# Optimization experiments

Hardware: AMD Instinct MI355X
Metric: run time of the kernel (lower is better)

Reference implementation:

```python
import jax, jax.numpy as jnp
import numpy as np

B = 512
INPUT_DIM = 1536
MAMBA_DIM = 1024
OUTPUT_DIM = 1024
D_STATE = 128
D_CONV = 4
EXPAND = 2
HEADDIM = 64
D_INNER = EXPAND * MAMBA_DIM          # 2048, == d_ssm
NHEADS = D_INNER // HEADDIM           # 32
CONV_DIM = D_INNER + 2 * D_STATE      # 2304
D_IN_PROJ = 2 * D_INNER + 2 * D_STATE + NHEADS  # 4384 (d_mlp = 0)
EPS = 1e-5


def rms_norm(x, g):
    return x * jax.lax.rsqrt(jnp.mean(x * x, axis=-1, keepdims=True) + EPS) * g


def setup_inputs() -> dict:
    key = jax.random.key(0)
    ks = jax.random.split(key, 16)
    def lin(k, fan_in, shape):
        return jax.random.normal(k, shape, jnp.float32) / np.sqrt(fan_in)
    return {
        "x": jax.random.normal(ks[0], (B, INPUT_DIM), jnp.float32),
        "conv_state": jax.random.normal(ks[1], (B, CONV_DIM, D_CONV), jnp.float32),
        "ssm_state": jax.random.normal(ks[2], (B, NHEADS, HEADDIM, D_STATE), jnp.float32),
        # NormedLinear in_proj (Linear + RMSNorm + SiLU)
        "w_in": lin(ks[3], INPUT_DIM, (INPUT_DIM, MAMBA_DIM)),
        "b_in": jnp.zeros((MAMBA_DIM,), jnp.float32),
        "g_in": jnp.ones((MAMBA_DIM,), jnp.float32),
        # Mamba2 params
        "W_inproj": lin(ks[4], MAMBA_DIM, (MAMBA_DIM, D_IN_PROJ)),
        "conv_w": lin(ks[5], D_CONV, (CONV_DIM, D_CONV)),
        "conv_b": jnp.zeros((CONV_DIM,), jnp.float32),
        "A_log": jnp.log(jax.random.uniform(ks[6], (NHEADS,), jnp.float32, 1.0, 16.0)),
        "dt_bias": 0.1 * jax.random.normal(ks[7], (NHEADS,), jnp.float32),
        "D": jnp.ones((NHEADS,), jnp.float32),
        "W_mamba_out": lin(ks[8], D_INNER, (D_INNER, MAMBA_DIM)),
        # outer out_proj Linear + RMSNorm
        "w_out": lin(ks[9], MAMBA_DIM, (MAMBA_DIM, OUTPUT_DIM)),
        "b_out": jnp.zeros((OUTPUT_DIM,), jnp.float32),
        "g_outnorm": jnp.ones((OUTPUT_DIM,), jnp.float32),
    }


def reference(x, conv_state, ssm_state, w_in, b_in, g_in, W_inproj, conv_w, conv_b,
              A_log, dt_bias, D, W_mamba_out, w_out, b_out, g_outnorm):
    # in_proj: Linear -> RMSNorm -> SiLU
    h = jax.nn.silu(rms_norm(x @ w_in + b_in, g_in))          # [B, MAMBA_DIM]
    zxbcdt = h @ W_inproj                                      # [B, D_IN_PROJ]
    z = zxbcdt[:, :D_INNER]                                    # [B, D_INNER]
    xbc = zxbcdt[:, D_INNER:D_INNER + CONV_DIM]                # [B, CONV_DIM]
    dt = zxbcdt[:, D_INNER + CONV_DIM:]                        # [B, NHEADS]
    # conv shift-and-sum
    conv_state_new = jnp.concatenate([conv_state[:, :, 1:], xbc[:, :, None]], axis=-1)
    xbc = jnp.sum(conv_state_new * conv_w[None], axis=-1) + conv_b
    xbc = jax.nn.silu(xbc)
    xh = xbc[:, :D_INNER].reshape(B, NHEADS, HEADDIM)          # [B, H, P]
    b = xbc[:, D_INNER:D_INNER + D_STATE]                      # [B, N]
    c = xbc[:, D_INNER + D_STATE:]                             # [B, N]
    # SSM step
    a = -jnp.exp(A_log)                                        # [H]
    dt = jax.nn.softplus(dt + dt_bias)                         # [B, H]
    da = jnp.exp(dt * a)                                       # [B, H]
    dbx = jnp.einsum('bh,bn,bhp->bhpn', dt, b, xh)
    ssm_state_new = ssm_state * da[:, :, None, None] + dbx     # [B, H, P, N]
    y = jnp.einsum('bhpn,bn->bhp', ssm_state_new, c)
    y = y + D[None, :, None] * xh
    y = y.reshape(B, D_INNER) * jax.nn.silu(z)
    y = y @ W_mamba_out                                        # [B, MAMBA_DIM]
    # outer projection + norm
    y = rms_norm(y @ w_out + b_out, g_outnorm)                 # [B, OUTPUT_DIM]
    return y, conv_state_new, ssm_state_new
```

## Files before the change

### kernel.cpp

```cpp
#include <hip/hip_runtime.h>
#include <hip/hip_bf16.h>

#define B_SZ      512
#define INPUT_DIM 1536
#define MAMBA_DIM 1024
#define OUT_DIM   1024
#define D_STATE   128
#define HEADDIM   64
#define D_INNER   2048
#define NHEADS    32
#define CONV_DIM  2304
#define D_IN_PROJ 4384

__device__ __forceinline__ float silu_precise(float x) {
    return x / (1.0f + expf(-x));
}

__global__ __launch_bounds__(256) void zero_kernel(float4* __restrict__ p, int n4)
{
    int i = blockIdx.x * 256 + threadIdx.x;
    const int stride = gridDim.x * 256;
    const float4 z = make_float4(0.f, 0.f, 0.f, 0.f);
    for (; i < n4; i += stride) p[i] = z;
}

__global__ __launch_bounds__(256) void sgemm_splitk_kernel(
    const float* __restrict__ A, const float* __restrict__ W,
    const float* __restrict__ bias, float* __restrict__ C,
    int M, int N, int K, int Kper)
{
    __shared__ float As[32][68];
    __shared__ float Bs[32][64];

    const int t   = threadIdx.x;
    const int bn0 = blockIdx.x * 64;
    const int bm0 = blockIdx.y * 64;
    const int kz0 = blockIdx.z * Kper;
    const int tr  = t >> 4;
    const int tc  = t & 15;

    float acc[4][4] = {};

    for (int kk = 0; kk < Kper; kk += 32) {
        const int k0 = kz0 + kk;
        #pragma unroll
        for (int i = 0; i < 2; ++i) {
            int idx = t + i * 256;
            int row = idx >> 3;
            int c4  = (idx & 7) * 4;
            float4 v = *(const float4*)(A + (size_t)(bm0 + row) * K + k0 + c4);
            As[c4 + 0][row] = v.x;
            As[c4 + 1][row] = v.y;
            As[c4 + 2][row] = v.z;
            As[c4 + 3][row] = v.w;
        }
        #pragma unroll
        for (int i = 0; i < 2; ++i) {
            int idx = t + i * 256;
            int kr  = idx >> 4;
            int c4  = (idx & 15) * 4;
            int n   = bn0 + c4;
            float4 v = make_float4(0.f, 0.f, 0.f, 0.f);
            if (n < N) v = *(const float4*)(W + (size_t)(k0 + kr) * N + n);
            *(float4*)&Bs[kr][c4] = v;
        }
        __syncthreads();

        #pragma unroll
        for (int k = 0; k < 32; ++k) {
            float4 a = *(const float4*)&As[k][tr * 4];
            float4 b = *(const float4*)&Bs[k][tc * 4];
            float av[4] = {a.x, a.y, a.z, a.w};
            float bv[4] = {b.x, b.y, b.z, b.w};
            #pragma unroll
            for (int i = 0; i < 4; ++i)
                #pragma unroll
                for (int j = 0; j < 4; ++j)
                    acc[i][j] += av[i] * bv[j];
        }
        __syncthreads();
    }

    const bool addb = (bias != nullptr) && (blockIdx.z == 0);
    #pragma unroll
    for (int i = 0; i < 4; ++i) {
        int m = bm0 + tr * 4 + i;
        #pragma unroll
        for (int j = 0; j < 4; ++j) {
            int n = bn0 + tc * 4 + j;
            if (n < N) {
                float v = acc[i][j];
                if (addb) v += bias[n];
                atomicAdd(&C[(size_t)m * N + n], v);
            }
        }
    }
}

template <bool SILU>
__global__ __launch_bounds__(256) void rmsnorm_kernel(
    const float* __restrict__ X, const float* __restrict__ g,
    float* __restrict__ Y)
{
    const int row = blockIdx.x;
    const float* x = X + (size_t)row * 1024;
    float4 v = *(const float4*)(x + threadIdx.x * 4);
    float ss = v.x * v.x + v.y * v.y + v.z * v.z + v.w * v.w;
    #pragma unroll
    for (int off = 32; off > 0; off >>= 1) ss += __shfl_down(ss, off);

    __shared__ float wsum[4];
    const int wid = threadIdx.x >> 6;
    if ((threadIdx.x & 63) == 0) wsum[wid] = ss;
    __syncthreads();
    const float tot = wsum[0] + wsum[1] + wsum[2] + wsum[3];
    const float rs = 1.0f / sqrtf(tot * (1.0f / 1024.0f) + 1e-5f);

    float4 gv = *(const float4*)(g + threadIdx.x * 4);
    float4 o;
    o.x = v.x * rs * gv.x;
    o.y = v.y * rs * gv.y;
    o.z = v.z * rs * gv.z;
    o.w = v.w * rs * gv.w;
    if (SILU) {
        o.x = silu_precise(o.x);
        o.y = silu_precise(o.y);
        o.z = silu_precise(o.z);
        o.w = silu_precise(o.w);
    }
    *(float4*)(Y + (size_t)row * 1024 + threadIdx.x * 4) = o;
}

__global__ __launch_bounds__(256) void conv_kernel(
    const float* __restrict__ conv_state, const float* __restrict__ zx,
    const float* __restrict__ conv_w, const float* __restrict__ conv_b,
    float* __restrict__ conv_state_out, float* __restrict__ xbc_out)
{
    const int gid = blockIdx.x * 256 + threadIdx.x;
    const int b = gid / CONV_DIM;
    const int c = gid - b * CONV_DIM;

    float4 cs = *(const float4*)(conv_state + (size_t)gid * 4);
    float xn = zx[(size_t)b * D_IN_PROJ + D_INNER + c];
    float4 w = *(const float4*)(conv_w + c * 4);

    float s = cs.y * w.x + cs.z * w.y + cs.w * w.z + xn * w.w + conv_b[c];
    float r = silu_precise(s);

    float4 o = make_float4(cs.y, cs.z, cs.w, xn);
    *(float4*)(conv_state_out + (size_t)gid * 4) = o;
    xbc_out[gid] = r;
}

__global__ __launch_bounds__(256) void ssm_kernel(
    const float* __restrict__ ssm_state, const float* __restrict__ xbc,
    const float* __restrict__ zx, const float* __restrict__ A_log,
    const float* __restrict__ dt_bias, const float* __restrict__ Dp,
    float* __restrict__ ssm_out, float* __restrict__ yz)
{
    const int h = blockIdx.x;
    const int b = blockIdx.y;
    const int t = threadIdx.x;
    const int lane_n = t & 31;
    const int n0 = lane_n * 4;
    const int pg = t >> 5;

    float dtv = zx[(size_t)b * D_IN_PROJ + (D_INNER + CONV_DIM) + h] + dt_bias[h];
    dtv = (dtv > 20.f) ? dtv : log1pf(expf(dtv));
    const float a  = -expf(A_log[h]);
    const float da = expf(dtv * a);
    const float dcoef = Dp[h];

    const float* xrow = xbc + (size_t)b * CONV_DIM;

    const float4 bb = *(const float4*)(xrow + D_INNER + n0);
    const float4 cc = *(const float4*)(xrow + D_INNER + D_STATE + n0);

    const size_t slab = ((size_t)b * NHEADS + h) * (HEADDIM * D_STATE);
    const float* sp = ssm_state + slab;
    float*       so = ssm_out   + slab;

    #pragma unroll
    for (int i = 0; i < 8; ++i) {
        const int p = pg + i * 8;
        const float xh = xrow[h * HEADDIM + p];
        const float coef = dtv * xh;

        const size_t off = (size_t)p * D_STATE + n0;
        float4 s = *(const float4*)(sp + off);
        float4 ns;
        ns.x = s.x * da + coef * bb.x;
        ns.y = s.y * da + coef * bb.y;
        ns.z = s.z * da + coef * bb.z;
        ns.w = s.w * da + coef * bb.w;
        *(float4*)(so + off) = ns;

        float y = ns.x * cc.x + ns.y * cc.y + ns.z * cc.z + ns.w * cc.w;
        y += __shfl_xor(y, 16);
        y += __shfl_xor(y, 8);
        y += __shfl_xor(y, 4);
        y += __shfl_xor(y, 2);
        y += __shfl_xor(y, 1);

        if (lane_n == 0) {
            float z = zx[(size_t)b * D_IN_PROJ + h * HEADDIM + p];
            float yv = y + dcoef * xh;
            yz[(size_t)b * D_INNER + h * HEADDIM + p] = yv * silu_precise(z);
        }
    }
}


extern "C" void kernel_launch(void* const* d_in, const int* in_sizes, int n_in,
                              void* d_out, int out_size, void* d_ws, size_t ws_size,
                              hipStream_t stream)
{
    const float* x          = (const float*)d_in[0];
    const float* conv_state = (const float*)d_in[1];
    const float* ssm_state  = (const float*)d_in[2];
    const float* w_in       = (const float*)d_in[3];
    const float* b_in       = (const float*)d_in[4];
    const float* g_in       = (const float*)d_in[5];
    const float* W_inproj   = (const float*)d_in[6];
    const float* conv_w     = (const float*)d_in[7];
    const float* conv_b     = (const float*)d_in[8];
    const float* A_log      = (const float*)d_in[9];
    const float* dt_bias    = (const float*)d_in[10];
    const float* Dp         = (const float*)d_in[11];
    const float* W_mamba_out= (const float*)d_in[12];
    const float* w_out      = (const float*)d_in[13];
    const float* b_out      = (const float*)d_in[14];
    const float* g_outnorm  = (const float*)d_in[15];

    float* out_y    = (float*)d_out;
    float* out_conv = out_y + (size_t)B_SZ * OUT_DIM;
    float* out_ssm  = out_conv + (size_t)B_SZ * CONV_DIM * 4;

    float* ws  = (float*)d_ws;
    float* t1  = ws;
    float* zx  = t1  + (size_t)B_SZ * MAMBA_DIM;
    float* u   = zx  + (size_t)B_SZ * D_IN_PROJ;
    float* t2  = u   + (size_t)B_SZ * MAMBA_DIM;
    float* h   = t2  + (size_t)B_SZ * MAMBA_DIM;
    float* xbc = h   + (size_t)B_SZ * MAMBA_DIM;
    float* yzb = xbc + (size_t)B_SZ * CONV_DIM;

    const int gemm_out_floats = B_SZ * (MAMBA_DIM + D_IN_PROJ + MAMBA_DIM + MAMBA_DIM);

    zero_kernel<<<2048, 256, 0, stream>>>((float4*)ws, gemm_out_floats / 4);

    sgemm_splitk_kernel<<<dim3(MAMBA_DIM / 64, B_SZ / 64, 8), 256, 0, stream>>>(
        x, w_in, b_in, t1, B_SZ, MAMBA_DIM, INPUT_DIM, INPUT_DIM / 8);
    rmsnorm_kernel<true><<<B_SZ, 256, 0, stream>>>(t1, g_in, h);
    sgemm_splitk_kernel<<<dim3((D_IN_PROJ + 63) / 64, B_SZ / 64, 4), 256, 0, stream>>>(
        h, W_inproj, nullptr, zx, B_SZ, D_IN_PROJ, MAMBA_DIM, MAMBA_DIM / 4);
    conv_kernel<<<(B_SZ * CONV_DIM) / 256, 256, 0, stream>>>(
        conv_state, zx, conv_w, conv_b, out_conv, xbc);
    ssm_kernel<<<dim3(NHEADS, B_SZ), 256, 0, stream>>>(
        ssm_state, xbc, zx, A_log, dt_bias, Dp, out_ssm, yzb);
    sgemm_splitk_kernel<<<dim3(MAMBA_DIM / 64, B_SZ / 64, 8), 256, 0, stream>>>(
        yzb, W_mamba_out, nullptr, u, B_SZ, MAMBA_DIM, D_INNER, D_INNER / 8);
    sgemm_splitk_kernel<<<dim3(OUT_DIM / 64, B_SZ / 64, 8), 256, 0, stream>>>(
        u, w_out, b_out, t2, B_SZ, OUT_DIM, MAMBA_DIM, MAMBA_DIM / 8);
    rmsnorm_kernel<false><<<B_SZ, 256, 0, stream>>>(t2, g_outnorm, out_y);
}
```

Before: 1.273 ms.

## Replace FP32 SIMT GEMMs with split-bf16x3 MFMA GEMMs on 128x128 tiles

Swaps the scalar FP32 split-K GEMM for a matrix-core kernel that splits each FP32 operand into bf16 hi/lo parts and uses three bf16 MFMAs per tile to approximate FP32 accuracy. Tiles grow from 64x64 to 128x128, with four waves each computing a 64x64 sub-tile. The aim is to move the four projection GEMMs from vector ALUs onto the MFMA units. In exchange, the hi/lo conversion adds ALU work, the B tile is stored transposed with scalar LDS writes that may cause bank conflicts, and the larger tiles give fewer blocks.

Result: faster. 1.102 ms (-13.4%).

```diff
diff --git a/kernel.cpp b/kernel.cpp
--- a/kernel.cpp
+++ b/kernel.cpp
@@ -1,5 +1,4 @@
 #include <hip/hip_runtime.h>
-#include <hip/hip_bf16.h>
 
 #define B_SZ      512
 #define INPUT_DIM 1536
@@ -12,8 +11,24 @@
 #define CONV_DIM  2304
 #define D_IN_PROJ 4384
 
+typedef short  short8 __attribute__((ext_vector_type(8)));
+typedef float  f32x4  __attribute__((ext_vector_type(4)));
+
 __device__ __forceinline__ float silu_precise(float x) {
     return x / (1.0f + expf(-x));
+}
+
+__device__ __forceinline__ ushort f2bf(float f) {
+    uint32_t u = __float_as_uint(f);
+    u += 0x7FFFu + ((u >> 16) & 1u);
+    return (ushort)(u >> 16);
+}
+__device__ __forceinline__ float bf2f(ushort h) {
+    return __uint_as_float(((uint32_t)h) << 16);
+}
+__device__ __forceinline__ void split_bf(float x, ushort& hi, ushort& lo) {
+    hi = f2bf(x);
+    lo = f2bf(x - bf2f(hi));
 }
 
 __global__ __launch_bounds__(256) void zero_kernel(float4* __restrict__ p, int n4)
@@ -24,74 +39,108 @@
     for (; i < n4; i += stride) p[i] = z;
 }
 
-__global__ __launch_bounds__(256) void sgemm_splitk_kernel(
+__global__ __launch_bounds__(256) void gemm_bf16x3_splitk(
     const float* __restrict__ A, const float* __restrict__ W,
     const float* __restrict__ bias, float* __restrict__ C,
     int M, int N, int K, int Kper)
 {
-    __shared__ float As[32][68];
-    __shared__ float Bs[32][64];
-
-    const int t   = threadIdx.x;
-    const int bn0 = blockIdx.x * 64;
-    const int bm0 = blockIdx.y * 64;
-    const int kz0 = blockIdx.z * Kper;
-    const int tr  = t >> 4;
-    const int tc  = t & 15;
-
-    float acc[4][4] = {};
+    __shared__ ushort As_hi[128][40];
+    __shared__ ushort As_lo[128][40];
+    __shared__ ushort Bs_hi[128][40];
+    __shared__ ushort Bs_lo[128][40];
+
+    const int t    = threadIdx.x;
+    const int bn0  = blockIdx.x * 128;
+    const int bm0  = blockIdx.y * 128;
+    const int kz0  = blockIdx.z * Kper;
+    const int wid  = t >> 6;
+    const int lane = t & 63;
+    const int wm   = (wid >> 1) * 64;
+    const int wn   = (wid & 1) * 64;
+    const int lr   = lane & 15;
+    const int lk   = lane >> 4;
+
+    f32x4 acc[4][4];
+    #pragma unroll
+    for (int i = 0; i < 4; ++i)
+        #pragma unroll
+        for (int j = 0; j < 4; ++j) {
+            f32x4 z = {0.f, 0.f, 0.f, 0.f};
+            acc[i][j] = z;
+        }
 
     for (int kk = 0; kk < Kper; kk += 32) {
         const int k0 = kz0 + kk;
-        #pragma unroll
-        for (int i = 0; i < 2; ++i) {
-            int idx = t + i * 256;
-            int row = idx >> 3;
-            int c4  = (idx & 7) * 4;
-            float4 v = *(const float4*)(A + (size_t)(bm0 + row) * K + k0 + c4);
-            As[c4 + 0][row] = v.x;
-            As[c4 + 1][row] = v.y;
-            As[c4 + 2][row] = v.z;
-            As[c4 + 3][row] = v.w;
-        }
-        #pragma unroll
-        for (int i = 0; i < 2; ++i) {
-            int idx = t + i * 256;
-            int kr  = idx >> 4;
-            int c4  = (idx & 15) * 4;
-            int n   = bn0 + c4;
+
+        #pragma unroll
+        for (int i = 0; i < 4; ++i) {
+            int c   = t + i * 256;
+            int row = c >> 3;
+            int k4  = (c & 7) * 4;
+            float4 v = *(const float4*)(A + (size_t)(bm0 + row) * K + k0 + k4);
+            ushort4 hi, lo;
+            split_bf(v.x, hi.x, lo.x);
+            split_bf(v.y, hi.y, lo.y);
+            split_bf(v.z, hi.z, lo.z);
+            split_bf(v.w, hi.w, lo.w);
+            *(ushort4*)&As_hi[row][k4] = hi;
+            *(ushort4*)&As_lo[row][k4] = lo;
+        }
+        #pragma unroll
+        for (int i = 0; i < 4; ++i) {
+            int c   = t + i * 256;
+            int kr  = c >> 5;
+            int n4  = (c & 31) * 4;
+            int n   = bn0 + n4;
             float4 v = make_float4(0.f, 0.f, 0.f, 0.f);
-            if (n < N) v = *(const float4*)(W + (size_t)(k0 + kr) * N + n);
-            *(float4*)&Bs[kr][c4] = v;
+            if (n + 4 <= N)
+                v = *(const float4*)(W + (size_t)(k0 + kr) * N + n);
+            ushort hi, lo;
+            split_bf(v.x, hi, lo); Bs_hi[n4 + 0][kr] = hi; Bs_lo[n4 + 0][kr] = lo;
+            split_bf(v.y, hi, lo); Bs_hi[n4 + 1][kr] = hi; Bs_lo[n4 + 1][kr] = lo;
+            split_bf(v.z, hi, lo); Bs_hi[n4 + 2][kr] = hi; Bs_lo[n4 + 2][kr] = lo;
+            split_bf(v.w, hi, lo); Bs_hi[n4 + 3][kr] = hi; Bs_lo[n4 + 3][kr] = lo;
         }
         __syncthreads();
 
-        #pragma unroll
-        for (int k = 0; k < 32; ++k) {
-            float4 a = *(const float4*)&As[k][tr * 4];
-            float4 b = *(const float4*)&Bs[k][tc * 4];
-            float av[4] = {a.x, a.y, a.z, a.w};
-            float bv[4] = {b.x, b.y, b.z, b.w};
+        short8 ah[4], al[4], bh[4], bl[4];
+        #pragma unroll
+        for (int mi = 0; mi < 4; ++mi) {
+            ah[mi] = *(const short8*)&As_hi[wm + mi * 16 + lr][lk * 8];
+            al[mi] = *(const short8*)&As_lo[wm + mi * 16 + lr][lk * 8];
+        }
+        #pragma unroll
+        for (int ni = 0; ni < 4; ++ni) {
+            bh[ni] = *(const short8*)&Bs_hi[wn + ni * 16 + lr][lk * 8];
+            bl[ni] = *(const short8*)&Bs_lo[wn + ni * 16 + lr][lk * 8];
+        }
+
+        #pragma unroll
+        for (int mi = 0; mi < 4; ++mi)
             #pragma unroll
-            for (int i = 0; i < 4; ++i)
-                #pragma unroll
-                for (int j = 0; j < 4; ++j)
-                    acc[i][j] += av[i] * bv[j];
-        }
+            for (int ni = 0; ni < 4; ++ni) {
+                f32x4 c0 = acc[mi][ni];
+                c0 = __builtin_amdgcn_mfma_f32_16x16x32_bf16(ah[mi], bh[ni], c0, 0, 0, 0);
+                c0 = __builtin_amdgcn_mfma_f32_16x16x32_bf16(ah[mi], bl[ni], c0, 0, 0, 0);
+                c0 = __builtin_amdgcn_mfma_f32_16x16x32_bf16(al[mi], bh[ni], c0, 0, 0, 0);
+                acc[mi][ni] = c0;
+            }
         __syncthreads();
     }
 
     const bool addb = (bias != nullptr) && (blockIdx.z == 0);
     #pragma unroll
-    for (int i = 0; i < 4; ++i) {
-        int m = bm0 + tr * 4 + i;
-        #pragma unroll
-        for (int j = 0; j < 4; ++j) {
-            int n = bn0 + tc * 4 + j;
-            if (n < N) {
-                float v = acc[i][j];
-                if (addb) v += bias[n];
-                atomicAdd(&C[(size_t)m * N + n], v);
+    for (int ni = 0; ni < 4; ++ni) {
+        int n = bn0 + wn + ni * 16 + lr;
+        if (n >= N) continue;
+        float bv = addb ? bias[n] : 0.f;
+        #pragma unroll
+        for (int mi = 0; mi < 4; ++mi) {
+            int mbase = bm0 + wm + mi * 16 + lk * 4;
+            #pragma unroll
+            for (int r = 0; r < 4; ++r) {
+                float v = acc[mi][ni][r] + bv;
+                atomicAdd(&C[(size_t)(mbase + r) * N + n], v);
             }
         }
     }
@@ -249,18 +298,18 @@
 
     zero_kernel<<<2048, 256, 0, stream>>>((float4*)ws, gemm_out_floats / 4);
 
-    sgemm_splitk_kernel<<<dim3(MAMBA_DIM / 64, B_SZ / 64, 8), 256, 0, stream>>>(
+    gemm_bf16x3_splitk<<<dim3(MAMBA_DIM / 128, B_SZ / 128, 8), 256, 0, stream>>>(
         x, w_in, b_in, t1, B_SZ, MAMBA_DIM, INPUT_DIM, INPUT_DIM / 8);
     rmsnorm_kernel<true><<<B_SZ, 256, 0, stream>>>(t1, g_in, h);
-    sgemm_splitk_kernel<<<dim3((D_IN_PROJ + 63) / 64, B_SZ / 64, 4), 256, 0, stream>>>(
+    gemm_bf16x3_splitk<<<dim3((D_IN_PROJ + 127) / 128, B_SZ / 128, 4), 256, 0, stream>>>(
         h, W_inproj, nullptr, zx, B_SZ, D_IN_PROJ, MAMBA_DIM, MAMBA_DIM / 4);
     conv_kernel<<<(B_SZ * CONV_DIM) / 256, 256, 0, stream>>>(
         conv_state, zx, conv_w, conv_b, out_conv, xbc);
     ssm_kernel<<<dim3(NHEADS, B_SZ), 256, 0, stream>>>(
         ssm_state, xbc, zx, A_log, dt_bias, Dp, out_ssm, yzb);
-    sgemm_splitk_kernel<<<dim3(MAMBA_DIM / 64, B_SZ / 64, 8), 256, 0, stream>>>(
+    gemm_bf16x3_splitk<<<dim3(MAMBA_DIM / 128, B_SZ / 128, 8), 256, 0, stream>>>(
         yzb, W_mamba_out, nullptr, u, B_SZ, MAMBA_DIM, D_INNER, D_INNER / 8);
-    sgemm_splitk_kernel<<<dim3(OUT_DIM / 64, B_SZ / 64, 8), 256, 0, stream>>>(
+    gemm_bf16x3_splitk<<<dim3(OUT_DIM / 128, B_SZ / 128, 8), 256, 0, stream>>>(
         u, w_out, b_out, t2, B_SZ, OUT_DIM, MAMBA_DIM, MAMBA_DIM / 8);
     rmsnorm_kernel<false><<<B_SZ, 256, 0, stream>>>(t2, g_outnorm, out_y);
 }
```
